# Optimization experiments

Hardware: AMD Instinct MI355X
Metric: run time of the kernel (lower is better)

## Reference

```python
import jax, jax.numpy as jnp
import numpy as np

HIDDEN = 4096


def setup_inputs() -> dict:
    key = jax.random.key(0)
    k1, k2 = jax.random.split(key)
    hidden_states = jax.random.normal(k1, (8, 2048, HIDDEN), dtype=jnp.float32)
    # gate_proj ~ N(0, 0.02^2), shape (2*hidden, hidden)
    gate_proj = 0.02 * jax.random.normal(k2, (2 * HIDDEN, HIDDEN), dtype=jnp.float32)
    return {"hidden_states": hidden_states, "gate_proj": gate_proj, "world_size": 8}


def reference(hidden_states, gate_proj, world_size):
    h = gate_proj.shape[1]
    view = hidden_states.reshape(-1, h)                 # [N, h]
    mm = jnp.einsum("nh,oh->no", view, gate_proj)      # [N, 2h]  (x @ W.T)
    n, o = mm.shape
    # reduce-scatter over dim 0 with world_size ranks: sum the per-rank chunks
    out = mm.reshape(world_size, n // world_size, o).sum(axis=0)  # [N/W, 2h]
    return out
```

## Files before the change

### kernel.cpp

```cpp
#include <hip/hip_runtime.h>
#include <hip/hip_bf16.h>


#define HID   4096
#define SEQ   2048
#define WORLD 8
#define OUTD  8192

typedef __bf16 bf16x8 __attribute__((ext_vector_type(8)));
typedef short  s16x8  __attribute__((ext_vector_type(8)));
typedef float  f32x4  __attribute__((ext_vector_type(4)));

typedef const __attribute__((address_space(1))) void* gas1_ptr;
typedef __attribute__((address_space(3))) void*       las3_ptr;

static __device__ __forceinline__ unsigned short f2bf(float f) {
    union { float f; unsigned u; } v; v.f = f;
    unsigned u = v.u;
    u += 0x7fffu + ((u >> 16) & 1u);
    return (unsigned short)(u >> 16);
}

#define RED_BLOCKS  2048
#define CONV_BLOCKS 4096
__global__ void prep_kernel(const float* __restrict__ hs,
                            const float* __restrict__ w,
                            unsigned short* __restrict__ xb,
                            unsigned short* __restrict__ wb) {
    if (blockIdx.x < RED_BLOCKS) {
        const int total4 = SEQ * HID / 4;
        const float4* h4 = (const float4*)hs;
        ushort4* o4 = (ushort4*)xb;
        for (int i = blockIdx.x * blockDim.x + threadIdx.x; i < total4;
             i += RED_BLOCKS * blockDim.x) {
            float4 s = h4[i];
            #pragma unroll
            for (int ww = 1; ww < WORLD; ++ww) {
                float4 t = h4[i + ww * total4];
                s.x += t.x; s.y += t.y; s.z += t.z; s.w += t.w;
            }
            ushort4 o;
            o.x = f2bf(s.x); o.y = f2bf(s.y); o.z = f2bf(s.z); o.w = f2bf(s.w);
            o4[i] = o;
        }
    } else {
        const int total4 = OUTD * HID / 4;
        const float4* w4 = (const float4*)w;
        ushort4* o4 = (ushort4*)wb;
        for (int i = (blockIdx.x - RED_BLOCKS) * blockDim.x + threadIdx.x;
             i < total4; i += CONV_BLOCKS * blockDim.x) {
            float4 s = w4[i];
            ushort4 o;
            o.x = f2bf(s.x); o.y = f2bf(s.y); o.z = f2bf(s.z); o.w = f2bf(s.w);
            o4[i] = o;
        }
    }
}


#define BM 256
#define BN 256
#define BK 64
#define KSTEPS (HID / BK)

__global__ __launch_bounds__(512, 2)
void gemm_bt_kernel(const unsigned short* __restrict__ A,
                    const unsigned short* __restrict__ B,
                    float* __restrict__ C) {
    __shared__ __align__(16) unsigned short lsA[2][BM * BK];
    __shared__ __align__(16) unsigned short lsB[2][BN * BK];

    const int tid  = threadIdx.x;
    const int lane = tid & 63;
    const int wave = tid >> 6;
    const int wm   = wave >> 2;
    const int wn   = wave & 3;

    const int bid   = blockIdx.x;
    const int xcd   = bid & 7;
    const int local = bid >> 3;
    const int bm = (xcd >> 2) * 4 + (local >> 3);
    const int bn = (xcd & 3) * 8 + (local & 7);

    const int subrow = lane >> 3;
    const int slot   = lane & 7;
    const int scol   = (slot ^ subrow) * 8;
    const unsigned short* aBase =
        A + (size_t)(bm * BM + wave * 8 + subrow) * HID + scol;
    const unsigned short* bBase =
        B + (size_t)(bn * BN + wave * 8 + subrow) * HID + scol;
    const int ldsW = wave * 8 * BK;

#define ST_A(buf, ktv, l) __builtin_amdgcn_global_load_lds(                     \
        (gas1_ptr)(aBase + (size_t)(ktv) * BK + (size_t)(l) * 64 * HID),        \
        (las3_ptr)(&lsA[buf][(l) * 64 * BK + ldsW]), 16, 0, 0)
#define ST_B(buf, ktv, l) __builtin_amdgcn_global_load_lds(                     \
        (gas1_ptr)(bBase + (size_t)(ktv) * BK + (size_t)(l) * 64 * HID),        \
        (las3_ptr)(&lsB[buf][(l) * 64 * BK + ldsW]), 16, 0, 0)

    const int fr    = lane & 15;
    const int fq    = lane >> 4;
    const int axor  = fr & 7;
    const int koff0 = ((0 + fq) ^ axor) * 8;
    const int koff1 = ((4 + fq) ^ axor) * 8;
    const int aRowB = (wm * 128 + fr) * BK;
    const int bRowB = (wn * 64 + fr) * BK;

#define RD_A(dst, p, mm, koff) dst = __builtin_bit_cast(bf16x8,                 \
        *(const s16x8*)&lsA[p][aRowB + (mm) * 16 * BK + (koff)])
#define RD_B(dst, p, nn, koff) dst = __builtin_bit_cast(bf16x8,                 \
        *(const s16x8*)&lsB[p][bRowB + (nn) * 16 * BK + (koff)])

#define BARRIER() __builtin_amdgcn_s_barrier()
#define LGKM0()   asm volatile("s_waitcnt lgkmcnt(0)" ::: "memory")
#define VMC8()    asm volatile("s_waitcnt vmcnt(8)" ::: "memory")
#define VMC0()    asm volatile("s_waitcnt vmcnt(0)" ::: "memory")
#define PRIO1()   __builtin_amdgcn_s_setprio(1)
#define PRIO0()   __builtin_amdgcn_s_setprio(0)

    f32x4 acc[8][4] = {};
    bf16x8 va[2][2], va2[2][2], vb[4][2];

    ST_A(0, 0, 0); ST_A(0, 0, 1); ST_A(0, 0, 2); ST_A(0, 0, 3);
    ST_B(0, 0, 0); ST_B(0, 0, 1); ST_B(0, 0, 2); ST_B(0, 0, 3);
    ST_A(1, 1, 0); ST_A(1, 1, 1); ST_A(1, 1, 2); ST_A(1, 1, 3);
    ST_B(1, 1, 0); ST_B(1, 1, 1); ST_B(1, 1, 2); ST_B(1, 1, 3);
    VMC8();
    BARRIER();

    for (int kt = 0; kt < KSTEPS; ++kt) {
        const int p = kt & 1;
        const bool st = (kt + 2 < KSTEPS);

        RD_B(vb[0][0], p, 0, koff0); RD_B(vb[0][1], p, 0, koff1);
        RD_B(vb[1][0], p, 1, koff0); RD_B(vb[1][1], p, 1, koff1);
        RD_B(vb[2][0], p, 2, koff0); RD_B(vb[2][1], p, 2, koff1);
        RD_B(vb[3][0], p, 3, koff0); RD_B(vb[3][1], p, 3, koff1);
        RD_A(va[0][0], p, 0, koff0); RD_A(va[0][1], p, 0, koff1);
        RD_A(va[1][0], p, 1, koff0); RD_A(va[1][1], p, 1, koff1);
        BARRIER();
        LGKM0();
        PRIO1();
        #pragma unroll
        for (int s = 0; s < 2; ++s)
            #pragma unroll
            for (int m = 0; m < 2; ++m)
                #pragma unroll
                for (int n = 0; n < 4; ++n)
                    acc[m][n] = __builtin_amdgcn_mfma_f32_16x16x32_bf16(
                        va[m][s], vb[n][s], acc[m][n], 0, 0, 0);
        PRIO0();
        BARRIER();

        RD_A(va[0][0], p, 2, koff0); RD_A(va[0][1], p, 2, koff1);
        RD_A(va[1][0], p, 3, koff0); RD_A(va[1][1], p, 3, koff1);
        if (st) { ST_B(p, kt + 2, 0); ST_B(p, kt + 2, 1);
                  ST_B(p, kt + 2, 2); ST_B(p, kt + 2, 3); }
        BARRIER();
        LGKM0();
        PRIO1();
        #pragma unroll
        for (int s = 0; s < 2; ++s)
            #pragma unroll
            for (int m = 0; m < 2; ++m)
                #pragma unroll
                for (int n = 0; n < 4; ++n)
                    acc[2 + m][n] = __builtin_amdgcn_mfma_f32_16x16x32_bf16(
                        va[m][s], vb[n][s], acc[2 + m][n], 0, 0, 0);
        PRIO0();
        BARRIER();

        RD_A(va[0][0],  p, 4, koff0); RD_A(va[0][1],  p, 4, koff1);
        RD_A(va[1][0],  p, 5, koff0); RD_A(va[1][1],  p, 5, koff1);
        RD_A(va2[0][0], p, 6, koff0); RD_A(va2[0][1], p, 6, koff1);
        RD_A(va2[1][0], p, 7, koff0); RD_A(va2[1][1], p, 7, koff1);
        BARRIER();
        LGKM0();
        PRIO1();
        #pragma unroll
        for (int s = 0; s < 2; ++s)
            #pragma unroll
            for (int m = 0; m < 2; ++m)
                #pragma unroll
                for (int n = 0; n < 4; ++n)
                    acc[4 + m][n] = __builtin_amdgcn_mfma_f32_16x16x32_bf16(
                        va[m][s], vb[n][s], acc[4 + m][n], 0, 0, 0);
        PRIO0();
        BARRIER();

        if (st) { ST_A(p, kt + 2, 0); ST_A(p, kt + 2, 1);
                  ST_A(p, kt + 2, 2); ST_A(p, kt + 2, 3); }
        BARRIER();
        PRIO1();
        #pragma unroll
        for (int s = 0; s < 2; ++s)
            #pragma unroll
            for (int m = 0; m < 2; ++m)
                #pragma unroll
                for (int n = 0; n < 4; ++n)
                    acc[6 + m][n] = __builtin_amdgcn_mfma_f32_16x16x32_bf16(
                        va2[m][s], vb[n][s], acc[6 + m][n], 0, 0, 0);
        PRIO0();
        if (st) { VMC8(); } else { VMC0(); }
        BARRIER();
    }

    const long crow0 = (long)bm * BM + wm * 128 + fq * 4;
    const long ccol0 = (long)bn * BN + wn * 64 + fr;
    #pragma unroll
    for (int m = 0; m < 8; ++m)
        #pragma unroll
        for (int n = 0; n < 4; ++n)
            #pragma unroll
            for (int j = 0; j < 4; ++j)
                C[(crow0 + m * 16 + j) * OUTD + ccol0 + n * 16] = acc[m][n][j];
}

extern "C" void kernel_launch(void* const* d_in, const int* in_sizes, int n_in,
                              void* d_out, int out_size, void* d_ws, size_t ws_size,
                              hipStream_t stream) {
    const float* hs = (const float*)d_in[0];
    const float* w  = (const float*)d_in[1];
    float* out = (float*)d_out;

    unsigned short* xb = (unsigned short*)d_ws;
    unsigned short* wb = xb + (size_t)SEQ * HID;

    hipLaunchKernelGGL(prep_kernel, dim3(RED_BLOCKS + CONV_BLOCKS), dim3(256),
                       0, stream, hs, w, xb, wb);
    hipLaunchKernelGGL(gemm_bt_kernel, dim3((SEQ / BM) * (OUTD / BN)), dim3(512),
                       0, stream, xb, wb, out);
}
```

Measured before the change: 235.1 us.

## Unroll K loop by two and spread global-to-LDS prefetches across phases

```diff
diff --git a/kernel.cpp b/kernel.cpp
--- a/kernel.cpp
+++ b/kernel.cpp
@@ -97,6 +97,8 @@
 #define ST_B(buf, ktv, l) __builtin_amdgcn_global_load_lds(                     \
         (gas1_ptr)(bBase + (size_t)(ktv) * BK + (size_t)(l) * 64 * HID),        \
         (las3_ptr)(&lsB[buf][(l) * 64 * BK + ldsW]), 16, 0, 0)
+#define STG_A(buf, ktv, h) do { ST_A(buf, ktv, 2*(h)); ST_A(buf, ktv, 2*(h)+1); } while (0)
+#define STG_B(buf, ktv, h) do { ST_B(buf, ktv, 2*(h)); ST_B(buf, ktv, 2*(h)+1); } while (0)
 
     const int fr    = lane & 15;
     const int fq    = lane >> 4;
@@ -106,102 +108,108 @@
     const int aRowB = (wm * 128 + fr) * BK;
     const int bRowB = (wn * 64 + fr) * BK;
 
-#define RD_A(dst, p, mm, koff) dst = __builtin_bit_cast(bf16x8,                 \
-        *(const s16x8*)&lsA[p][aRowB + (mm) * 16 * BK + (koff)])
-#define RD_B(dst, p, nn, koff) dst = __builtin_bit_cast(bf16x8,                 \
-        *(const s16x8*)&lsB[p][bRowB + (nn) * 16 * BK + (koff)])
+#define RD_A(dst, P, mm, koff) dst = __builtin_bit_cast(bf16x8,                 \
+        *(const s16x8*)&lsA[P][aRowB + (mm) * 16 * BK + (koff)])
+#define RD_B(dst, P, nn, koff) dst = __builtin_bit_cast(bf16x8,                 \
+        *(const s16x8*)&lsB[P][bRowB + (nn) * 16 * BK + (koff)])
 
 #define BARRIER() __builtin_amdgcn_s_barrier()
 #define LGKM0()   asm volatile("s_waitcnt lgkmcnt(0)" ::: "memory")
-#define VMC8()    asm volatile("s_waitcnt vmcnt(8)" ::: "memory")
+#define LGKM8()   asm volatile("s_waitcnt lgkmcnt(8)" ::: "memory")
+#define VMC6()    asm volatile("s_waitcnt vmcnt(6)" ::: "memory")
 #define VMC0()    asm volatile("s_waitcnt vmcnt(0)" ::: "memory")
 #define PRIO1()   __builtin_amdgcn_s_setprio(1)
 #define PRIO0()   __builtin_amdgcn_s_setprio(0)
 
+#define MFMA16(VAx, mb)                                                          \
+    PRIO1();                                                                     \
+    _Pragma("unroll")                                                            \
+    for (int s = 0; s < 2; ++s)                                                  \
+        _Pragma("unroll")                                                        \
+        for (int m = 0; m < 2; ++m)                                              \
+            _Pragma("unroll")                                                    \
+            for (int n = 0; n < 4; ++n)                                          \
+                acc[(mb) + m][n] = __builtin_amdgcn_mfma_f32_16x16x32_bf16(      \
+                    VAx[m][s], vb[n][s], acc[(mb) + m][n], 0, 0, 0);             \
+    PRIO0()
+
+#define READS_PH_FIRST(P)                                                        \
+    RD_B(vb[0][0], P, 0, koff0); RD_B(vb[0][1], P, 0, koff1);                    \
+    RD_B(vb[1][0], P, 1, koff0); RD_B(vb[1][1], P, 1, koff1);                    \
+    RD_B(vb[2][0], P, 2, koff0); RD_B(vb[2][1], P, 2, koff1);                    \
+    RD_B(vb[3][0], P, 3, koff0); RD_B(vb[3][1], P, 3, koff1);                    \
+    RD_A(va[0][0], P, 0, koff0); RD_A(va[0][1], P, 0, koff1);                    \
+    RD_A(va[1][0], P, 1, koff0); RD_A(va[1][1], P, 1, koff1)
+
     f32x4 acc[8][4] = {};
     bf16x8 va[2][2], va2[2][2], vb[4][2];
 
-    ST_A(0, 0, 0); ST_A(0, 0, 1); ST_A(0, 0, 2); ST_A(0, 0, 3);
-    ST_B(0, 0, 0); ST_B(0, 0, 1); ST_B(0, 0, 2); ST_B(0, 0, 3);
-    ST_A(1, 1, 0); ST_A(1, 1, 1); ST_A(1, 1, 2); ST_A(1, 1, 3);
-    ST_B(1, 1, 0); ST_B(1, 1, 1); ST_B(1, 1, 2); ST_B(1, 1, 3);
-    VMC8();
+    STG_B(0, 0, 0); STG_B(0, 0, 1); STG_A(0, 0, 0); STG_A(0, 0, 1);
+    STG_B(1, 1, 0); STG_B(1, 1, 1); STG_A(1, 1, 0);
+    VMC6();
     BARRIER();
 
-    for (int kt = 0; kt < KSTEPS; ++kt) {
-        const int p = kt & 1;
-        const bool st = (kt + 2 < KSTEPS);
-
-        RD_B(vb[0][0], p, 0, koff0); RD_B(vb[0][1], p, 0, koff1);
-        RD_B(vb[1][0], p, 1, koff0); RD_B(vb[1][1], p, 1, koff1);
-        RD_B(vb[2][0], p, 2, koff0); RD_B(vb[2][1], p, 2, koff1);
-        RD_B(vb[3][0], p, 3, koff0); RD_B(vb[3][1], p, 3, koff1);
-        RD_A(va[0][0], p, 0, koff0); RD_A(va[0][1], p, 0, koff1);
-        RD_A(va[1][0], p, 1, koff0); RD_A(va[1][1], p, 1, koff1);
-        BARRIER();
-        LGKM0();
-        PRIO1();
-        #pragma unroll
-        for (int s = 0; s < 2; ++s)
-            #pragma unroll
-            for (int m = 0; m < 2; ++m)
-                #pragma unroll
-                for (int n = 0; n < 4; ++n)
-                    acc[m][n] = __builtin_amdgcn_mfma_f32_16x16x32_bf16(
-                        va[m][s], vb[n][s], acc[m][n], 0, 0, 0);
-        PRIO0();
-        BARRIER();
-
-        RD_A(va[0][0], p, 2, koff0); RD_A(va[0][1], p, 2, koff1);
-        RD_A(va[1][0], p, 3, koff0); RD_A(va[1][1], p, 3, koff1);
-        if (st) { ST_B(p, kt + 2, 0); ST_B(p, kt + 2, 1);
-                  ST_B(p, kt + 2, 2); ST_B(p, kt + 2, 3); }
-        BARRIER();
-        LGKM0();
-        PRIO1();
-        #pragma unroll
-        for (int s = 0; s < 2; ++s)
-            #pragma unroll
-            for (int m = 0; m < 2; ++m)
-                #pragma unroll
-                for (int n = 0; n < 4; ++n)
-                    acc[2 + m][n] = __builtin_amdgcn_mfma_f32_16x16x32_bf16(
-                        va[m][s], vb[n][s], acc[2 + m][n], 0, 0, 0);
-        PRIO0();
-        BARRIER();
-
-        RD_A(va[0][0],  p, 4, koff0); RD_A(va[0][1],  p, 4, koff1);
-        RD_A(va[1][0],  p, 5, koff0); RD_A(va[1][1],  p, 5, koff1);
-        RD_A(va2[0][0], p, 6, koff0); RD_A(va2[0][1], p, 6, koff1);
-        RD_A(va2[1][0], p, 7, koff0); RD_A(va2[1][1], p, 7, koff1);
-        BARRIER();
-        LGKM0();
-        PRIO1();
-        #pragma unroll
-        for (int s = 0; s < 2; ++s)
-            #pragma unroll
-            for (int m = 0; m < 2; ++m)
-                #pragma unroll
-                for (int n = 0; n < 4; ++n)
-                    acc[4 + m][n] = __builtin_amdgcn_mfma_f32_16x16x32_bf16(
-                        va[m][s], vb[n][s], acc[4 + m][n], 0, 0, 0);
-        PRIO0();
-        BARRIER();
-
-        if (st) { ST_A(p, kt + 2, 0); ST_A(p, kt + 2, 1);
-                  ST_A(p, kt + 2, 2); ST_A(p, kt + 2, 3); }
-        BARRIER();
-        PRIO1();
-        #pragma unroll
-        for (int s = 0; s < 2; ++s)
-            #pragma unroll
-            for (int m = 0; m < 2; ++m)
-                #pragma unroll
-                for (int n = 0; n < 4; ++n)
-                    acc[6 + m][n] = __builtin_amdgcn_mfma_f32_16x16x32_bf16(
-                        va2[m][s], vb[n][s], acc[6 + m][n], 0, 0, 0);
-        PRIO0();
-        if (st) { VMC8(); } else { VMC0(); }
+    #pragma unroll 1
+    for (int t = 0; t < KSTEPS; t += 2) {
+        const bool st2 = (t + 2 < KSTEPS);
+        const bool st3 = (t + 3 < KSTEPS);
+
+        READS_PH_FIRST(0);
+        STG_A(1, t + 1, 1);
+        LGKM8();
+        BARRIER(); LGKM0();
+        MFMA16(va, 0);
+        BARRIER();
+
+        RD_A(va[0][0], 0, 2, koff0); RD_A(va[0][1], 0, 2, koff1);
+        RD_A(va[1][0], 0, 3, koff0); RD_A(va[1][1], 0, 3, koff1);
+        if (st2) STG_B(0, t + 2, 0);
+        BARRIER(); LGKM0();
+        MFMA16(va, 2);
+        BARRIER();
+
+        RD_A(va[0][0],  0, 4, koff0); RD_A(va[0][1],  0, 4, koff1);
+        RD_A(va[1][0],  0, 5, koff0); RD_A(va[1][1],  0, 5, koff1);
+        RD_A(va2[0][0], 0, 6, koff0); RD_A(va2[0][1], 0, 6, koff1);
+        RD_A(va2[1][0], 0, 7, koff0); RD_A(va2[1][1], 0, 7, koff1);
+        if (st2) STG_B(0, t + 2, 1);
+        BARRIER(); LGKM0();
+        MFMA16(va, 4);
+        BARRIER();
+
+        if (st2) STG_A(0, t + 2, 0);
+        BARRIER();
+        MFMA16(va2, 6);
+        if (st2) { VMC6(); } else { VMC0(); }
+        BARRIER();
+
+        READS_PH_FIRST(1);
+        if (st2) STG_A(0, t + 2, 1);
+        LGKM8();
+        BARRIER(); LGKM0();
+        MFMA16(va, 0);
+        BARRIER();
+
+        RD_A(va[0][0], 1, 2, koff0); RD_A(va[0][1], 1, 2, koff1);
+        RD_A(va[1][0], 1, 3, koff0); RD_A(va[1][1], 1, 3, koff1);
+        if (st3) STG_B(1, t + 3, 0);
+        BARRIER(); LGKM0();
+        MFMA16(va, 2);
+        BARRIER();
+
+        RD_A(va[0][0],  1, 4, koff0); RD_A(va[0][1],  1, 4, koff1);
+        RD_A(va[1][0],  1, 5, koff0); RD_A(va[1][1],  1, 5, koff1);
+        RD_A(va2[0][0], 1, 6, koff0); RD_A(va2[0][1], 1, 6, koff1);
+        RD_A(va2[1][0], 1, 7, koff0); RD_A(va2[1][1], 1, 7, koff1);
+        if (st3) STG_B(1, t + 3, 1);
+        BARRIER(); LGKM0();
+        MFMA16(va, 4);
+        BARRIER();
+
+        if (st3) STG_A(1, t + 3, 0);
+        BARRIER();
+        MFMA16(va2, 6);
+        if (st3) { VMC6(); } else { VMC0(); }
         BARRIER();
     }
 
```

After: 223.0 us. 1.05x faster.
